# Optimization experiments

Measured on AMD Instinct MI355X. Metric: run time of the kernel, lower is better.

The kernel has to match this reference:

```python
import jax, jax.numpy as jnp
import numpy as np

B, C, W, H = 16, 512, 32, 32


def spatial_shift1(y):
    # y: [B, W, H, C]; quartile-wise shifts with edge rows/cols left unchanged
    c = y.shape[-1]
    cq = c // 4
    p0 = jnp.concatenate([y[:, :1, :, 0*cq:1*cq], y[:, :-1, :, 0*cq:1*cq]], axis=1)  # w <- w-1
    p1 = jnp.concatenate([y[:, 1:, :, 1*cq:2*cq], y[:, -1:, :, 1*cq:2*cq]], axis=1)  # w <- w+1
    p2 = jnp.concatenate([y[:, :, :1, 2*cq:3*cq], y[:, :, :-1, 2*cq:3*cq]], axis=2)  # h <- h-1
    p3 = jnp.concatenate([y[:, :, 1:, 3*cq:], y[:, :, -1:, 3*cq:]], axis=2)          # h <- h+1
    return jnp.concatenate([p0, p1, p2, p3], axis=-1)


def spatial_shift2(y):
    # same as shift1 with w/h roles swapped
    c = y.shape[-1]
    cq = c // 4
    p0 = jnp.concatenate([y[:, :, :1, 0*cq:1*cq], y[:, :, :-1, 0*cq:1*cq]], axis=2)  # h <- h-1
    p1 = jnp.concatenate([y[:, :, 1:, 1*cq:2*cq], y[:, :, -1:, 1*cq:2*cq]], axis=2)  # h <- h+1
    p2 = jnp.concatenate([y[:, :1, :, 2*cq:3*cq], y[:, :-1, :, 2*cq:3*cq]], axis=1)  # w <- w-1
    p3 = jnp.concatenate([y[:, 1:, :, 3*cq:], y[:, -1:, :, 3*cq:]], axis=1)          # w <- w+1
    return jnp.concatenate([p0, p1, p2, p3], axis=-1)


def setup_inputs() -> dict:
    key = jax.random.key(0)
    ks = jax.random.split(key, 9)
    s = 0.02
    return {
        "x": jax.random.normal(ks[0], (B, C, W, H), dtype=jnp.float32),
        "w1": jax.random.normal(ks[1], (3 * C, C), dtype=jnp.float32) * s,
        "b1": jax.random.normal(ks[2], (3 * C,), dtype=jnp.float32) * s,
        "wa": jax.random.normal(ks[3], (C, C), dtype=jnp.float32) * s,
        "ba": jax.random.normal(ks[4], (C,), dtype=jnp.float32) * s,
        "wb": jax.random.normal(ks[5], (3 * C, C), dtype=jnp.float32) * s,
        "bb": jax.random.normal(ks[6], (3 * C,), dtype=jnp.float32) * s,
        "w2": jax.random.normal(ks[7], (C, C), dtype=jnp.float32) * s,
        "b2": jax.random.normal(ks[8], (C,), dtype=jnp.float32) * s,
    }


def reference(x, w1, b1, wa, ba, wb, bb, w2, b2):
    c = x.shape[1]
    xp = jnp.transpose(x, (0, 2, 3, 1))                     # [B, W, H, C]
    y = jnp.einsum("bwhc,oc->bwho", xp, w1) + b1            # [B, W, H, 3C]
    x1 = spatial_shift1(y[..., :c])
    x2 = spatial_shift2(y[..., c:2 * c])
    x3 = y[..., 2 * c:]
    # SplitAttention: descriptor a = sum over branches and spatial positions
    a = jnp.sum(x1 + x2 + x3, axis=(1, 2))                  # [B, C]
    hat = jax.nn.gelu(a @ wa.T + ba, approximate=False) @ wb.T + bb  # [B, 3C]
    bar = jax.nn.softmax(hat.reshape(-1, 3, c), axis=1)     # softmax over k=3
    g = bar[:, :, None, None, :]                            # [B, 3, 1, 1, C]
    out = g[:, 0] * x1 + g[:, 1] * x2 + g[:, 2] * x3        # [B, W, H, C]
    z = jnp.einsum("bwhc,oc->bwho", out, w2) + b2           # [B, W, H, C]
    return jnp.transpose(z, (0, 3, 1, 2))                   # [B, C, W, H]
```

## Files before the change

### kernel.cpp

```cpp
#include <hip/hip_runtime.h>
#include <stdint.h>

typedef __bf16 bf16x8 __attribute__((ext_vector_type(8)));
typedef float f32x4 __attribute__((ext_vector_type(4)));

#define B_ 16
#define C_ 512
#define S_ 1024
#define N1 1536

__device__ inline unsigned short f2b(float f) {
    unsigned int u = __builtin_bit_cast(unsigned int, f);
    unsigned int lsb = (u >> 16) & 1u;
    u += 0x7fffu + lsb;
    return (unsigned short)(u >> 16);
}
__device__ inline float b2f(unsigned int s) {
    unsigned int u = (s & 0xffffu) << 16;
    return __builtin_bit_cast(float, u);
}

__device__ inline void gl_lds16(const unsigned short* g, unsigned short* l) {
    __builtin_amdgcn_global_load_lds(
        (const __attribute__((address_space(1))) void*)(g),
        (__attribute__((address_space(3))) void*)(l),
        16, 0, 0);
}

__global__ void transpose_convert_x(const float* __restrict__ x, unsigned short* __restrict__ xT,
                                    const float* __restrict__ w1, const float* __restrict__ w2,
                                    unsigned short* __restrict__ w1b, unsigned short* __restrict__ w2b,
                                    float* __restrict__ sums) {
    if (blockIdx.z == 16) {
        int t = (blockIdx.y * 32 + blockIdx.x) * 256 + threadIdx.y * 32 + threadIdx.x;
#pragma unroll
        for (int it = 0; it < 3; it++) {
            int i = t + it * 131072;
            if (i < 196608) {
                float4 v = ((const float4*)w1)[i];
                ((ushort4*)w1b)[i] = make_ushort4(f2b(v.x), f2b(v.y), f2b(v.z), f2b(v.w));
            } else if (i < 262144) {
                int j = i - 196608;
                float4 v = ((const float4*)w2)[j];
                ((ushort4*)w2b)[j] = make_ushort4(f2b(v.x), f2b(v.y), f2b(v.z), f2b(v.w));
            } else if (i < 292864) {
                int j = i - 262144;
                ((float4*)sums)[j] = make_float4(0.f, 0.f, 0.f, 0.f);
            }
        }
        return;
    }
    __shared__ float tile[32][33];
    int b = blockIdx.z;
    int c0 = blockIdx.y * 32;
    int s0 = blockIdx.x * 32;
    int tx = threadIdx.x, ty = threadIdx.y;
    const float* xp = x + ((size_t)b * C_ + c0) * S_ + s0;
#pragma unroll
    for (int i = 0; i < 4; i++)
        tile[ty + i * 8][tx] = xp[(size_t)(ty + i * 8) * S_ + tx];
    __syncthreads();
    unsigned short* op = xT + ((size_t)b * S_ + s0) * C_ + c0;
#pragma unroll
    for (int i = 0; i < 4; i++)
        op[(size_t)(ty + i * 8) * C_ + tx] = f2b(tile[tx][ty + i * 8]);
}

template <bool TRANS_OUT, bool DO_SUMS>
__global__ __launch_bounds__(512, 2) void gemm_2ph(
    const unsigned short* __restrict__ A,
    const unsigned short* __restrict__ Wt,
    const float* __restrict__ bias,
    void* __restrict__ Cout,
    float* __restrict__ Tsum, float* __restrict__ H0, float* __restrict__ H31,
    float* __restrict__ C0, float* __restrict__ C31)
{
    __shared__ __align__(16) unsigned short lds[49152];
    const int tid = threadIdx.x;
    const int lane = tid & 63, wid = tid >> 6;
    const int wm = (wid >> 2) * 64;
    const int wn = (wid & 3) * 64;
    const int quad = lane >> 4, l16 = lane & 15;
    const int m0 = blockIdx.x * 128;
    const int n0 = blockIdx.y * 256;
    const unsigned short* Ab = A + (size_t)m0 * 512;
    const unsigned short* Bb = Wt + (size_t)n0 * 512;

    f32x4 acc[4][4] = {};

    auto stageA = [&](int T) {
        unsigned short* dst = &lds[(T & 1) * 8192];
#pragma unroll
        for (int i = 0; i < 2; i++) {
            int ch = i * 512 + tid;
            int r = ch >> 3, kc = ch & 7;
            gl_lds16(Ab + (size_t)r * 512 + T * 64 + ((kc ^ (r & 7)) * 8), dst + ch * 8);
        }
    };
    auto stageB = [&](int T) {
        unsigned short* dst = &lds[16384 + (T & 1) * 16384];
#pragma unroll
        for (int i = 0; i < 4; i++) {
            int ch = i * 512 + tid;
            int r = ch >> 3, kc = ch & 7;
            gl_lds16(Bb + (size_t)r * 512 + T * 64 + ((kc ^ (r & 7)) * 8), dst + ch * 8);
        }
    };

    stageB(0); stageA(0); stageB(1);
    asm volatile("s_waitcnt vmcnt(4)" ::: "memory");
    __builtin_amdgcn_s_barrier();

    for (int T = 0; T < 8; T++) {
        const unsigned short* Asl = &lds[(T & 1) * 8192];
        const unsigned short* Bsl = &lds[16384 + (T & 1) * 16384];
        bf16x8 bfr[4][2], af[2][2];
#pragma unroll
        for (int nt = 0; nt < 4; nt++)
#pragma unroll
            for (int kh = 0; kh < 2; kh++) {
                int rb = wn + nt * 16 + l16;
                bfr[nt][kh] = *(const bf16x8*)&Bsl[rb * 64 + (((kh * 4 + quad) ^ (rb & 7)) * 8)];
            }
#pragma unroll
        for (int mi = 0; mi < 2; mi++)
#pragma unroll
            for (int kh = 0; kh < 2; kh++) {
                int ra = wm + mi * 16 + l16;
                af[mi][kh] = *(const bf16x8*)&Asl[ra * 64 + (((kh * 4 + quad) ^ (ra & 7)) * 8)];
            }
        if (T < 7) stageA(T + 1);
        __builtin_amdgcn_s_barrier();
        asm volatile("s_waitcnt lgkmcnt(0)" ::: "memory");
        __builtin_amdgcn_sched_barrier(0);
        __builtin_amdgcn_s_setprio(1);
#pragma unroll
        for (int mi = 0; mi < 2; mi++)
#pragma unroll
            for (int nt = 0; nt < 4; nt++)
#pragma unroll
                for (int kh = 0; kh < 2; kh++)
                    acc[mi][nt] = __builtin_amdgcn_mfma_f32_16x16x32_bf16(
                        af[mi][kh], bfr[nt][kh], acc[mi][nt], 0, 0, 0);
        __builtin_amdgcn_s_setprio(0);
        __builtin_amdgcn_s_barrier();
#pragma unroll
        for (int mi = 0; mi < 2; mi++)
#pragma unroll
            for (int kh = 0; kh < 2; kh++) {
                int ra = wm + (2 + mi) * 16 + l16;
                af[mi][kh] = *(const bf16x8*)&Asl[ra * 64 + (((kh * 4 + quad) ^ (ra & 7)) * 8)];
            }
        if (T < 6) {
            stageB(T + 2);
            asm volatile("s_waitcnt vmcnt(4)" ::: "memory");
        } else if (T == 6) {
            asm volatile("s_waitcnt vmcnt(0)" ::: "memory");
        }
        __builtin_amdgcn_s_barrier();
        asm volatile("s_waitcnt lgkmcnt(0)" ::: "memory");
        __builtin_amdgcn_sched_barrier(0);
        __builtin_amdgcn_s_setprio(1);
#pragma unroll
        for (int mi = 0; mi < 2; mi++)
#pragma unroll
            for (int nt = 0; nt < 4; nt++)
#pragma unroll
                for (int kh = 0; kh < 2; kh++)
                    acc[2 + mi][nt] = __builtin_amdgcn_mfma_f32_16x16x32_bf16(
                        af[mi][kh], bfr[nt][kh], acc[2 + mi][nt], 0, 0, 0);
        __builtin_amdgcn_s_setprio(0);
        __builtin_amdgcn_s_barrier();
    }

    if (!TRANS_OUT) {
        unsigned short* eb = lds;
#pragma unroll
        for (int mt = 0; mt < 4; mt++)
#pragma unroll
            for (int nt = 0; nt < 4; nt++) {
                int col = wn + nt * 16 + l16;
                float bv = bias[n0 + col];
                int cc = col >> 3, cw = col & 7;
#pragma unroll
                for (int r = 0; r < 4; r++) {
                    int row = wm + mt * 16 + quad * 4 + r;
                    eb[row * 256 + (((cc ^ (row & 7)) << 3) + cw)] = f2b(acc[mt][nt][r] + bv);
                }
            }
        __syncthreads();
        unsigned short* Y = (unsigned short*)Cout;
#pragma unroll
        for (int it = 0; it < 8; it++) {
            int cid = it * 512 + tid;
            int row = cid >> 5, j = cid & 31;
            bf16x8 v = *(const bf16x8*)&eb[row * 256 + ((j ^ (row & 7)) << 3)];
            *(bf16x8*)&Y[(size_t)(m0 + row) * N1 + n0 + j * 8] = v;
        }
    } else {
        float* ef = (float*)lds;
        int b = m0 >> 10, s0r = m0 & 1023;
        float* O = (float*)Cout;
#pragma unroll
        for (int p = 0; p < 2; p++) {
            if (((wid & 3) >> 1) == p) {
#pragma unroll
                for (int mt = 0; mt < 4; mt++)
#pragma unroll
                    for (int nt = 0; nt < 4; nt++) {
                        int nl = wn - p * 128 + nt * 16 + l16;
                        float bv = bias[n0 + p * 128 + nl];
                        int c = (wm >> 2) + mt * 4 + quad;
                        f32x4 v;
#pragma unroll
                        for (int r = 0; r < 4; r++) v[r] = acc[mt][nt][r] + bv;
                        *(f32x4*)&ef[nl * 128 + ((c ^ (nl & 7)) << 2)] = v;
                    }
            }
            __syncthreads();
#pragma unroll
            for (int it = 0; it < 8; it++) {
                int cid = it * 512 + tid;
                int nl = cid >> 5, j = cid & 31;
                f32x4 v = *(const f32x4*)&ef[nl * 128 + ((j ^ (nl & 7)) << 2)];
                *(f32x4*)&O[((size_t)(b * 512 + n0 + p * 128 + nl)) * 1024 + s0r + j * 4] = v;
            }
            if (p == 0) __syncthreads();
        }
    }

    if (DO_SUMS) {
        int b = m0 >> 10;
        int wlo = (m0 & 1023) >> 5;
#pragma unroll
        for (int nt = 0; nt < 4; nt++) {
            int n = n0 + wn + nt * 16 + l16;
            float bv = bias[n];
            float tT = 0.f;
#pragma unroll
            for (int mt = 0; mt < 4; mt++)
#pragma unroll
                for (int r = 0; r < 4; r++) tT += acc[mt][nt][r] + bv;
            tT += __shfl_xor(tT, 16);
            tT += __shfl_xor(tT, 32);
            if (quad == 0) {
                atomicAdd(&Tsum[b * 1536 + n], tT);
                float th0 = acc[0][nt][0] + acc[2][nt][0] + 2.f * bv;
                atomicAdd(&H0[b * 1536 + n], th0);
            }
            if (quad == 3) {
                float th31 = acc[1][nt][3] + acc[3][nt][3] + 2.f * bv;
                atomicAdd(&H31[b * 1536 + n], th31);
            }
            if (wlo == 0 && wm == 0) {
                float tc = 0.f;
#pragma unroll
                for (int mt = 0; mt < 2; mt++)
#pragma unroll
                    for (int r = 0; r < 4; r++) tc += acc[mt][nt][r] + bv;
                tc += __shfl_xor(tc, 16);
                tc += __shfl_xor(tc, 32);
                if (quad == 0) atomicAdd(&C0[b * 1536 + n], tc);
            }
            if (wlo == 28 && wm == 64) {
                float tc = 0.f;
#pragma unroll
                for (int mt = 2; mt < 4; mt++)
#pragma unroll
                    for (int r = 0; r < 4; r++) tc += acc[mt][nt][r] + bv;
                tc += __shfl_xor(tc, 16);
                tc += __shfl_xor(tc, 32);
                if (quad == 0) atomicAdd(&C31[b * 1536 + n], tc);
            }
        }
    }
}

__global__ __launch_bounds__(256) void mlp_layer1(
    const float* __restrict__ sums, const float* __restrict__ wa,
    const float* __restrict__ ba, float* __restrict__ h)
{
    __shared__ float sa[512];
    int b = blockIdx.x >> 7;
    int t = threadIdx.x;
    const float* Tp   = sums;
    const float* H0p  = sums + 24576;
    const float* H31p = sums + 49152;
    const float* C0p  = sums + 73728;
    const float* C31p = sums + 98304;
#pragma unroll
    for (int j = 0; j < 2; j++) {
        int c = t + j * 256;
        int q = c >> 7;
        int n1 = b * 1536 + c;
        float t123 = Tp[n1] + Tp[n1 + 512] + Tp[n1 + 1024];
        float sC1 = C0p[n1] - C31p[n1];
        float sH1 = H0p[n1] - H31p[n1];
        float sC2 = C0p[n1 + 512] - C31p[n1 + 512];
        float sH2 = H0p[n1 + 512] - H31p[n1 + 512];
        float e = (q < 2) ? (sC1 + sH2) : (sH1 + sC2);
        sa[c] = t123 + ((q & 1) ? -e : e);
    }
    __syncthreads();
    int lane = t & 63, wid = t >> 6;
    int o = (blockIdx.x & 127) * 4 + wid;
    const float4* wr = (const float4*)(wa + (size_t)o * 512);
    float4 w0 = wr[lane * 2], w1v = wr[lane * 2 + 1];
    float4 a0 = ((const float4*)sa)[lane * 2], a1 = ((const float4*)sa)[lane * 2 + 1];
    float dot = w0.x * a0.x + w0.y * a0.y + w0.z * a0.z + w0.w * a0.w
              + w1v.x * a1.x + w1v.y * a1.y + w1v.z * a1.z + w1v.w * a1.w;
#pragma unroll
    for (int off = 32; off; off >>= 1) dot += __shfl_down(dot, off);
    if (lane == 0) {
        float v = dot + ba[o];
        h[b * 512 + o] = 0.5f * v * (1.0f + erff(v * 0.7071067811865475f));
    }
}

__global__ __launch_bounds__(256) void mlp_layer2(
    const float* __restrict__ h, const float* __restrict__ wb,
    const float* __restrict__ bb, float* __restrict__ hat)
{
    int gw = (blockIdx.x * 256 + threadIdx.x) >> 6;
    int lane = threadIdx.x & 63;
    int b = gw / 1536;
    int o = gw - b * 1536;
    const float4* wr = (const float4*)(wb + (size_t)o * 512);
    const float4* hr = (const float4*)(h + (size_t)b * 512);
    float4 w0 = wr[lane * 2], w1 = wr[lane * 2 + 1];
    float4 h0 = hr[lane * 2], h1 = hr[lane * 2 + 1];
    float dot = w0.x * h0.x + w0.y * h0.y + w0.z * h0.z + w0.w * h0.w
              + w1.x * h1.x + w1.y * h1.y + w1.z * h1.z + w1.w * h1.w;
#pragma unroll
    for (int off = 32; off; off >>= 1) dot += __shfl_down(dot, off);
    if (lane == 0)
        hat[(size_t)b * 1536 + o] = dot + bb[o];
}

__global__ __launch_bounds__(256) void combine_softmax(
    const unsigned short* __restrict__ y, const float* __restrict__ hat,
    unsigned short* __restrict__ outT)
{
    int b = blockIdx.y;
    int w = blockIdx.x;
    int t = threadIdx.x;
    int h0 = (t >> 6) * 8;
    int c8 = (t & 63) * 8;
    int q = c8 >> 7;
    int dw1 = (q == 0) ? -1 : (q == 1) ? 1 : 0;
    int dh1 = (q == 2) ? -1 : (q == 3) ? 1 : 0;
    int dh2 = (q == 0) ? -1 : (q == 1) ? 1 : 0;
    int dw2 = (q == 2) ? -1 : (q == 3) ? 1 : 0;
    float g0[8], g1[8], g2[8];
#pragma unroll
    for (int j = 0; j < 8; j++) {
        int c = c8 + j;
        float h0v = hat[b * 1536 + c];
        float h1v = hat[b * 1536 + 512 + c];
        float h2v = hat[b * 1536 + 1024 + c];
        float mx = fmaxf(h0v, fmaxf(h1v, h2v));
        float e0 = __expf(h0v - mx), e1 = __expf(h1v - mx), e2 = __expf(h2v - mx);
        float inv = 1.0f / (e0 + e1 + e2);
        g0[j] = e0 * inv; g1[j] = e1 * inv; g2[j] = e2 * inv;
    }
    int w1i = min(max(w + dw1, 0), 31);
    int w2i = min(max(w + dw2, 0), 31);
    size_t base = (size_t)b * S_;
#pragma unroll
    for (int hh = 0; hh < 8; hh++) {
        int h = h0 + hh;
        int h1i = min(max(h + dh1, 0), 31);
        int h2i = min(max(h + dh2, 0), 31);
        uint4 u1 = *(const uint4*)&y[(base + w1i * 32 + h1i) * N1 + c8];
        uint4 u2 = *(const uint4*)&y[(base + w2i * 32 + h2i) * N1 + 512 + c8];
        uint4 u3 = *(const uint4*)&y[(base + w * 32 + h) * N1 + 1024 + c8];
        unsigned int p[4];
        const unsigned int* a1 = &u1.x;
        const unsigned int* a2 = &u2.x;
        const unsigned int* a3 = &u3.x;
#pragma unroll
        for (int k = 0; k < 4; k++) {
            int j = k * 2;
            float lo = g0[j] * b2f(a1[k]) + g1[j] * b2f(a2[k]) + g2[j] * b2f(a3[k]);
            float hi = g0[j + 1] * b2f(a1[k] >> 16) + g1[j + 1] * b2f(a2[k] >> 16) + g2[j + 1] * b2f(a3[k] >> 16);
            p[k] = (unsigned int)f2b(lo) | ((unsigned int)f2b(hi) << 16);
        }
        *(uint4*)&outT[(base + w * 32 + h) * 512 + c8] = make_uint4(p[0], p[1], p[2], p[3]);
    }
}

extern "C" void kernel_launch(void* const* d_in, const int* in_sizes, int n_in,
                              void* d_out, int out_size, void* d_ws, size_t ws_size,
                              hipStream_t stream) {
    const float* x  = (const float*)d_in[0];
    const float* w1 = (const float*)d_in[1];
    const float* b1 = (const float*)d_in[2];
    const float* wa = (const float*)d_in[3];
    const float* ba = (const float*)d_in[4];
    const float* wb = (const float*)d_in[5];
    const float* bb = (const float*)d_in[6];
    const float* w2 = (const float*)d_in[7];
    const float* b2 = (const float*)d_in[8];
    float* out = (float*)d_out;

    char* ws = (char*)d_ws;
    unsigned short* xT   = (unsigned short*)(ws);
    unsigned short* outT = (unsigned short*)(ws);
    unsigned short* w1b  = (unsigned short*)(ws + 16777216);
    unsigned short* w2b  = (unsigned short*)(ws + 18350080);
    unsigned short* y    = (unsigned short*)(ws + 18874368);
    float* sums          = (float*)(ws + 69206016);
    float* h_buf         = (float*)(ws + 69697536);
    float* hat_buf       = (float*)(ws + 69730304);

    float* Tsum = sums;
    float* H0   = sums + 24576;
    float* H31  = sums + 49152;
    float* C0   = sums + 73728;
    float* C31  = sums + 98304;

    transpose_convert_x<<<dim3(32, 16, 17), dim3(32, 8), 0, stream>>>(
        x, xT, w1, w2, w1b, w2b, sums);
    gemm_2ph<false, true><<<dim3(128, 6), dim3(512), 0, stream>>>(
        xT, w1b, b1, (void*)y, Tsum, H0, H31, C0, C31);
    mlp_layer1<<<dim3(2048), dim3(256), 0, stream>>>(sums, wa, ba, h_buf);
    mlp_layer2<<<dim3(6144), dim3(256), 0, stream>>>(h_buf, wb, bb, hat_buf);
    combine_softmax<<<dim3(32, 16), dim3(256), 0, stream>>>(y, hat_buf, outT);
    gemm_2ph<true, false><<<dim3(128, 2), dim3(512), 0, stream>>>(
        outT, w2b, b2, (void*)out, nullptr, nullptr, nullptr, nullptr, nullptr);
}
```

Baseline: 177.3 us.

## Fuse softmax-weighted shift combine into second GEMM A-operand load

Removes the separate combine_softmax kernel and its bf16 outT round trip. The new gemm2_fused kernel computes the softmax gates per block and gathers the shifted y rows directly into its LDS A tile, double-buffered with the B staging. Separately, the x transpose now uses 64x64 tiles with vectorized float4 loads and 16-byte stores. mlp_layer2 computes four outputs per wave with h cached in shared memory. The cost is that each of the two N-blocks now repeats the gather and blend work, and the A-loads run on the GEMM's critical path.

```diff
diff --git a/kernel.cpp b/kernel.cpp
--- a/kernel.cpp
+++ b/kernel.cpp
@@ -27,15 +27,16 @@
         16, 0, 0);
 }
 
-__global__ void transpose_convert_x(const float* __restrict__ x, unsigned short* __restrict__ xT,
-                                    const float* __restrict__ w1, const float* __restrict__ w2,
-                                    unsigned short* __restrict__ w1b, unsigned short* __restrict__ w2b,
-                                    float* __restrict__ sums) {
+__global__ __launch_bounds__(256) void transpose_convert_x(
+    const float* __restrict__ x, unsigned short* __restrict__ xT,
+    const float* __restrict__ w1, const float* __restrict__ w2,
+    unsigned short* __restrict__ w1b, unsigned short* __restrict__ w2b,
+    float* __restrict__ sums)
+{
+    int t = threadIdx.x;
     if (blockIdx.z == 16) {
-        int t = (blockIdx.y * 32 + blockIdx.x) * 256 + threadIdx.y * 32 + threadIdx.x;
-#pragma unroll
-        for (int it = 0; it < 3; it++) {
-            int i = t + it * 131072;
+        int base = (blockIdx.y * 16 + blockIdx.x) * 256 + t;
+        for (int i = base; i < 292864; i += 32768) {
             if (i < 196608) {
                 float4 v = ((const float4*)w1)[i];
                 ((ushort4*)w1b)[i] = make_ushort4(f2b(v.x), f2b(v.y), f2b(v.z), f2b(v.w));
@@ -43,27 +44,38 @@
                 int j = i - 196608;
                 float4 v = ((const float4*)w2)[j];
                 ((ushort4*)w2b)[j] = make_ushort4(f2b(v.x), f2b(v.y), f2b(v.z), f2b(v.w));
-            } else if (i < 292864) {
+            } else {
                 int j = i - 262144;
                 ((float4*)sums)[j] = make_float4(0.f, 0.f, 0.f, 0.f);
             }
         }
         return;
     }
-    __shared__ float tile[32][33];
+    __shared__ float tile[64][68];
     int b = blockIdx.z;
-    int c0 = blockIdx.y * 32;
-    int s0 = blockIdx.x * 32;
-    int tx = threadIdx.x, ty = threadIdx.y;
-    const float* xp = x + ((size_t)b * C_ + c0) * S_ + s0;
-#pragma unroll
-    for (int i = 0; i < 4; i++)
-        tile[ty + i * 8][tx] = xp[(size_t)(ty + i * 8) * S_ + tx];
+    int c0 = blockIdx.y * 64;
+    int s0 = blockIdx.x * 64;
+    int r = t >> 2, q4 = t & 3;
+    const float* xp = x + ((size_t)(b * C_ + c0 + r)) * S_ + s0;
+#pragma unroll
+    for (int k = 0; k < 4; k++) {
+        float4 v = ((const float4*)xp)[q4 + 4 * k];
+        *(float4*)&tile[r][(q4 + 4 * k) * 4] = v;
+    }
     __syncthreads();
-    unsigned short* op = xT + ((size_t)b * S_ + s0) * C_ + c0;
-#pragma unroll
-    for (int i = 0; i < 4; i++)
-        op[(size_t)(ty + i * 8) * C_ + tx] = f2b(tile[tx][ty + i * 8]);
+    int sr = t >> 2;
+    unsigned short* op = xT + ((size_t)(b * S_ + s0 + sr)) * C_ + c0;
+#pragma unroll
+    for (int kk = 0; kk < 2; kk++) {
+        int chunk = q4 + 4 * kk;
+        unsigned int pz[4];
+#pragma unroll
+        for (int i2 = 0; i2 < 4; i2++) {
+            int c = chunk * 8 + i2 * 2;
+            pz[i2] = (unsigned int)f2b(tile[c][sr]) | ((unsigned int)f2b(tile[c + 1][sr]) << 16);
+        }
+        *(uint4*)&op[chunk * 8] = make_uint4(pz[0], pz[1], pz[2], pz[3]);
+    }
 }
 
 template <bool TRANS_OUT, bool DO_SUMS>
@@ -276,6 +288,198 @@
     }
 }
 
+__global__ __launch_bounds__(512, 2) void gemm2_fused(
+    const unsigned short* __restrict__ Yg,
+    const float* __restrict__ hat,
+    const unsigned short* __restrict__ Wt,
+    const float* __restrict__ bias,
+    float* __restrict__ O)
+{
+    __shared__ __align__(16) unsigned short As[2 * 8192];
+    __shared__ __align__(16) unsigned short Bs[2 * 16384];
+    __shared__ float gs[3][512];
+    const int tid = threadIdx.x;
+    const int lane = tid & 63, wid = tid >> 6;
+    const int wm = (wid >> 2) * 64;
+    const int wn = (wid & 3) * 64;
+    const int quad = lane >> 4, l16 = lane & 15;
+    const int m0 = blockIdx.x * 128;
+    const int n0 = blockIdx.y * 256;
+    const int b = m0 >> 10, s0 = m0 & 1023, w0 = s0 >> 5;
+    const int bq = b * 1024;
+    const unsigned short* Bb = Wt + (size_t)n0 * 512;
+    const int chunk = tid & 7, mpair = tid >> 3;
+    const int wA = w0 + ((mpair * 2) >> 5);
+
+    f32x4 acc[4][4] = {};
+
+    {
+        int c = tid;
+        float h0v = hat[b * 1536 + c];
+        float h1v = hat[b * 1536 + 512 + c];
+        float h2v = hat[b * 1536 + 1024 + c];
+        float mx = fmaxf(h0v, fmaxf(h1v, h2v));
+        float e0 = __expf(h0v - mx), e1 = __expf(h1v - mx), e2 = __expf(h2v - mx);
+        float inv = 1.0f / (e0 + e1 + e2);
+        gs[0][c] = e0 * inv; gs[1][c] = e1 * inv; gs[2][c] = e2 * inv;
+    }
+    __syncthreads();
+
+    auto stageB = [&](int T) {
+        unsigned short* dst = &Bs[(T & 1) * 16384];
+#pragma unroll
+        for (int i = 0; i < 4; i++) {
+            int ch = i * 512 + tid;
+            int r = ch >> 3, kc = ch & 7;
+            gl_lds16(Bb + (size_t)r * 512 + T * 64 + ((kc ^ (r & 7)) * 8), dst + ch * 8);
+        }
+    };
+
+    uint4 u1[2], u2[2], u3[2];
+    auto issueA = [&](int Tn) {
+        int q = Tn >> 1;
+        int dw1 = (q == 0) ? -1 : (q == 1) ? 1 : 0;
+        int dh1 = (q == 2) ? -1 : (q == 3) ? 1 : 0;
+        int dh2 = (q == 0) ? -1 : (q == 1) ? 1 : 0;
+        int dw2 = (q == 2) ? -1 : (q == 3) ? 1 : 0;
+        int cg = Tn * 64 + chunk * 8;
+#pragma unroll
+        for (int j = 0; j < 2; j++) {
+            int ml = mpair * 2 + j;
+            int w = w0 + (ml >> 5), h = ml & 31;
+            int r1 = bq + min(max(w + dw1, 0), 31) * 32 + min(max(h + dh1, 0), 31);
+            int r2 = bq + min(max(w + dw2, 0), 31) * 32 + min(max(h + dh2, 0), 31);
+            int r3 = bq + w * 32 + h;
+            u1[j] = *(const uint4*)&Yg[(size_t)r1 * 1536 + cg];
+            u2[j] = *(const uint4*)&Yg[(size_t)r2 * 1536 + 512 + cg];
+            u3[j] = *(const uint4*)&Yg[(size_t)r3 * 1536 + 1024 + cg];
+        }
+    };
+    auto writeA = [&](int Tn) {
+        int cg = Tn * 64 + chunk * 8;
+        float g0v[8], g1v[8], g2v[8];
+        *(float4*)&g0v[0] = *(const float4*)&gs[0][cg];
+        *(float4*)&g0v[4] = *(const float4*)&gs[0][cg + 4];
+        *(float4*)&g1v[0] = *(const float4*)&gs[1][cg];
+        *(float4*)&g1v[4] = *(const float4*)&gs[1][cg + 4];
+        *(float4*)&g2v[0] = *(const float4*)&gs[2][cg];
+        *(float4*)&g2v[4] = *(const float4*)&gs[2][cg + 4];
+#pragma unroll
+        for (int j = 0; j < 2; j++) {
+            const unsigned int* a1 = (const unsigned int*)&u1[j];
+            const unsigned int* a2 = (const unsigned int*)&u2[j];
+            const unsigned int* a3 = (const unsigned int*)&u3[j];
+            unsigned int p[4];
+#pragma unroll
+            for (int k = 0; k < 4; k++) {
+                float lo = g0v[2 * k] * b2f(a1[k]) + g1v[2 * k] * b2f(a2[k]) + g2v[2 * k] * b2f(a3[k]);
+                float hi = g0v[2 * k + 1] * b2f(a1[k] >> 16) + g1v[2 * k + 1] * b2f(a2[k] >> 16) + g2v[2 * k + 1] * b2f(a3[k] >> 16);
+                p[k] = (unsigned int)f2b(lo) | ((unsigned int)f2b(hi) << 16);
+            }
+            int ml = mpair * 2 + j;
+            *(uint4*)&As[(Tn & 1) * 8192 + ml * 64 + ((chunk ^ (ml & 7)) * 8)] = *(const uint4*)p;
+        }
+    };
+
+    stageB(0);
+    issueA(0);
+    stageB(1);
+    asm volatile("s_waitcnt vmcnt(4)" ::: "memory");
+    writeA(0);
+    asm volatile("s_waitcnt lgkmcnt(0)" ::: "memory");
+    __builtin_amdgcn_s_barrier();
+
+    for (int T = 0; T < 8; T++) {
+        const unsigned short* Asl = &As[(T & 1) * 8192];
+        const unsigned short* Bsl = &Bs[(T & 1) * 16384];
+        bf16x8 bfr[4][2], af[2][2];
+#pragma unroll
+        for (int nt = 0; nt < 4; nt++)
+#pragma unroll
+            for (int kh = 0; kh < 2; kh++) {
+                int rb = wn + nt * 16 + l16;
+                bfr[nt][kh] = *(const bf16x8*)&Bsl[rb * 64 + (((kh * 4 + quad) ^ (rb & 7)) * 8)];
+            }
+#pragma unroll
+        for (int mi = 0; mi < 2; mi++)
+#pragma unroll
+            for (int kh = 0; kh < 2; kh++) {
+                int ra = wm + mi * 16 + l16;
+                af[mi][kh] = *(const bf16x8*)&Asl[ra * 64 + (((kh * 4 + quad) ^ (ra & 7)) * 8)];
+            }
+        if (T < 7) issueA(T + 1);
+        __builtin_amdgcn_s_barrier();
+        asm volatile("s_waitcnt lgkmcnt(0)" ::: "memory");
+        __builtin_amdgcn_sched_barrier(0);
+        __builtin_amdgcn_s_setprio(1);
+#pragma unroll
+        for (int mi = 0; mi < 2; mi++)
+#pragma unroll
+            for (int nt = 0; nt < 4; nt++)
+#pragma unroll
+                for (int kh = 0; kh < 2; kh++)
+                    acc[mi][nt] = __builtin_amdgcn_mfma_f32_16x16x32_bf16(
+                        af[mi][kh], bfr[nt][kh], acc[mi][nt], 0, 0, 0);
+        __builtin_amdgcn_s_setprio(0);
+        __builtin_amdgcn_s_barrier();
+#pragma unroll
+        for (int mi = 0; mi < 2; mi++)
+#pragma unroll
+            for (int kh = 0; kh < 2; kh++) {
+                int ra = wm + (2 + mi) * 16 + l16;
+                af[mi][kh] = *(const bf16x8*)&Asl[ra * 64 + (((kh * 4 + quad) ^ (ra & 7)) * 8)];
+            }
+        if (T < 6) stageB(T + 2);
+        if (T < 7) {
+            if (T < 6) asm volatile("s_waitcnt vmcnt(4)" ::: "memory");
+            else       asm volatile("s_waitcnt vmcnt(0)" ::: "memory");
+            writeA(T + 1);
+        }
+        __builtin_amdgcn_s_barrier();
+        asm volatile("s_waitcnt lgkmcnt(0)" ::: "memory");
+        __builtin_amdgcn_sched_barrier(0);
+        __builtin_amdgcn_s_setprio(1);
+#pragma unroll
+        for (int mi = 0; mi < 2; mi++)
+#pragma unroll
+            for (int nt = 0; nt < 4; nt++)
+#pragma unroll
+                for (int kh = 0; kh < 2; kh++)
+                    acc[2 + mi][nt] = __builtin_amdgcn_mfma_f32_16x16x32_bf16(
+                        af[mi][kh], bfr[nt][kh], acc[2 + mi][nt], 0, 0, 0);
+        __builtin_amdgcn_s_setprio(0);
+        __builtin_amdgcn_s_barrier();
+    }
+
+    float* ef = (float*)Bs;
+#pragma unroll
+    for (int p = 0; p < 2; p++) {
+        if (((wid & 3) >> 1) == p) {
+#pragma unroll
+            for (int mt = 0; mt < 4; mt++)
+#pragma unroll
+                for (int nt = 0; nt < 4; nt++) {
+                    int nl = wn - p * 128 + nt * 16 + l16;
+                    float bv = bias[n0 + p * 128 + nl];
+                    int c = (wm >> 2) + mt * 4 + quad;
+                    f32x4 v;
+#pragma unroll
+                    for (int r = 0; r < 4; r++) v[r] = acc[mt][nt][r] + bv;
+                    *(f32x4*)&ef[nl * 128 + ((c ^ (nl & 7)) << 2)] = v;
+                }
+        }
+        __syncthreads();
+#pragma unroll
+        for (int it = 0; it < 8; it++) {
+            int cid = it * 512 + tid;
+            int nl = cid >> 5, j = cid & 31;
+            f32x4 v = *(const f32x4*)&ef[nl * 128 + ((j ^ (nl & 7)) << 2)];
+            *(f32x4*)&O[((size_t)(b * 512 + n0 + p * 128 + nl)) * 1024 + s0 + j * 4] = v;
+        }
+        if (p == 0) __syncthreads();
+    }
+}
+
 __global__ __launch_bounds__(256) void mlp_layer1(
     const float* __restrict__ sums, const float* __restrict__ wa,
     const float* __restrict__ ba, float* __restrict__ h)
@@ -321,71 +525,26 @@
     const float* __restrict__ h, const float* __restrict__ wb,
     const float* __restrict__ bb, float* __restrict__ hat)
 {
-    int gw = (blockIdx.x * 256 + threadIdx.x) >> 6;
-    int lane = threadIdx.x & 63;
-    int b = gw / 1536;
-    int o = gw - b * 1536;
-    const float4* wr = (const float4*)(wb + (size_t)o * 512);
-    const float4* hr = (const float4*)(h + (size_t)b * 512);
-    float4 w0 = wr[lane * 2], w1 = wr[lane * 2 + 1];
-    float4 h0 = hr[lane * 2], h1 = hr[lane * 2 + 1];
-    float dot = w0.x * h0.x + w0.y * h0.y + w0.z * h0.z + w0.w * h0.w
-              + w1.x * h1.x + w1.y * h1.y + w1.z * h1.z + w1.w * h1.w;
-#pragma unroll
-    for (int off = 32; off; off >>= 1) dot += __shfl_down(dot, off);
-    if (lane == 0)
-        hat[(size_t)b * 1536 + o] = dot + bb[o];
-}
-
-__global__ __launch_bounds__(256) void combine_softmax(
-    const unsigned short* __restrict__ y, const float* __restrict__ hat,
-    unsigned short* __restrict__ outT)
-{
-    int b = blockIdx.y;
-    int w = blockIdx.x;
+    __shared__ float sh[512];
+    int b = blockIdx.x / 96;
+    int og = blockIdx.x - b * 96;
     int t = threadIdx.x;
-    int h0 = (t >> 6) * 8;
-    int c8 = (t & 63) * 8;
-    int q = c8 >> 7;
-    int dw1 = (q == 0) ? -1 : (q == 1) ? 1 : 0;
-    int dh1 = (q == 2) ? -1 : (q == 3) ? 1 : 0;
-    int dh2 = (q == 0) ? -1 : (q == 1) ? 1 : 0;
-    int dw2 = (q == 2) ? -1 : (q == 3) ? 1 : 0;
-    float g0[8], g1[8], g2[8];
-#pragma unroll
-    for (int j = 0; j < 8; j++) {
-        int c = c8 + j;
-        float h0v = hat[b * 1536 + c];
-        float h1v = hat[b * 1536 + 512 + c];
-        float h2v = hat[b * 1536 + 1024 + c];
-        float mx = fmaxf(h0v, fmaxf(h1v, h2v));
-        float e0 = __expf(h0v - mx), e1 = __expf(h1v - mx), e2 = __expf(h2v - mx);
-        float inv = 1.0f / (e0 + e1 + e2);
-        g0[j] = e0 * inv; g1[j] = e1 * inv; g2[j] = e2 * inv;
-    }
-    int w1i = min(max(w + dw1, 0), 31);
-    int w2i = min(max(w + dw2, 0), 31);
-    size_t base = (size_t)b * S_;
-#pragma unroll
-    for (int hh = 0; hh < 8; hh++) {
-        int h = h0 + hh;
-        int h1i = min(max(h + dh1, 0), 31);
-        int h2i = min(max(h + dh2, 0), 31);
-        uint4 u1 = *(const uint4*)&y[(base + w1i * 32 + h1i) * N1 + c8];
-        uint4 u2 = *(const uint4*)&y[(base + w2i * 32 + h2i) * N1 + 512 + c8];
-        uint4 u3 = *(const uint4*)&y[(base + w * 32 + h) * N1 + 1024 + c8];
-        unsigned int p[4];
-        const unsigned int* a1 = &u1.x;
-        const unsigned int* a2 = &u2.x;
-        const unsigned int* a3 = &u3.x;
-#pragma unroll
-        for (int k = 0; k < 4; k++) {
-            int j = k * 2;
-            float lo = g0[j] * b2f(a1[k]) + g1[j] * b2f(a2[k]) + g2[j] * b2f(a3[k]);
-            float hi = g0[j + 1] * b2f(a1[k] >> 16) + g1[j + 1] * b2f(a2[k] >> 16) + g2[j + 1] * b2f(a3[k] >> 16);
-            p[k] = (unsigned int)f2b(lo) | ((unsigned int)f2b(hi) << 16);
-        }
-        *(uint4*)&outT[(base + w * 32 + h) * 512 + c8] = make_uint4(p[0], p[1], p[2], p[3]);
+    sh[t] = h[b * 512 + t];
+    sh[t + 256] = h[b * 512 + 256 + t];
+    __syncthreads();
+    int lane = t & 63, wid = t >> 6;
+    float4 a0 = ((const float4*)sh)[lane * 2], a1 = ((const float4*)sh)[lane * 2 + 1];
+#pragma unroll
+    for (int i = 0; i < 4; i++) {
+        int o = og * 16 + wid * 4 + i;
+        const float4* wr = (const float4*)(wb + (size_t)o * 512);
+        float4 w0 = wr[lane * 2], w1 = wr[lane * 2 + 1];
+        float dot = w0.x * a0.x + w0.y * a0.y + w0.z * a0.z + w0.w * a0.w
+                  + w1.x * a1.x + w1.y * a1.y + w1.z * a1.z + w1.w * a1.w;
+#pragma unroll
+        for (int off = 32; off; off >>= 1) dot += __shfl_down(dot, off);
+        if (lane == 0)
+            hat[(size_t)b * 1536 + o] = dot + bb[o];
     }
 }
 
@@ -405,7 +564,6 @@
 
     char* ws = (char*)d_ws;
     unsigned short* xT   = (unsigned short*)(ws);
-    unsigned short* outT = (unsigned short*)(ws);
     unsigned short* w1b  = (unsigned short*)(ws + 16777216);
     unsigned short* w2b  = (unsigned short*)(ws + 18350080);
     unsigned short* y    = (unsigned short*)(ws + 18874368);
@@ -419,13 +577,12 @@
     float* C0   = sums + 73728;
     float* C31  = sums + 98304;
 
-    transpose_convert_x<<<dim3(32, 16, 17), dim3(32, 8), 0, stream>>>(
+    transpose_convert_x<<<dim3(16, 8, 17), dim3(256), 0, stream>>>(
         x, xT, w1, w2, w1b, w2b, sums);
     gemm_2ph<false, true><<<dim3(128, 6), dim3(512), 0, stream>>>(
         xT, w1b, b1, (void*)y, Tsum, H0, H31, C0, C31);
     mlp_layer1<<<dim3(2048), dim3(256), 0, stream>>>(sums, wa, ba, h_buf);
-    mlp_layer2<<<dim3(6144), dim3(256), 0, stream>>>(h_buf, wb, bb, hat_buf);
-    combine_softmax<<<dim3(32, 16), dim3(256), 0, stream>>>(y, hat_buf, outT);
-    gemm_2ph<true, false><<<dim3(128, 2), dim3(512), 0, stream>>>(
-        outT, w2b, b2, (void*)out, nullptr, nullptr, nullptr, nullptr, nullptr);
-}
+    mlp_layer2<<<dim3(1536), dim3(256), 0, stream>>>(h_buf, wb, bb, hat_buf);
+    gemm2_fused<<<dim3(128, 2), dim3(512), 0, stream>>>(
+        y, hat_buf, w2b, b2, out);
+}
```

Measured after the change: 175.3 us. No clear change (-1.1%).
